# Kernel tuning notes

Measured on AMD Instinct MI355X. Metric: run time of the kernel, lower is better.

The kernel has to match this reference:

```python
import jax, jax.numpy as jnp
import numpy as np

T, B, D, H, NQ = 512, 256, 256, 256, 4  # note H == B is required by the original torch broadcasting


def setup_inputs() -> dict:
    key = jax.random.key(0)
    ks = jax.random.split(key, 9)
    inp = {"inputs": jax.random.normal(ks[0], (T, B, D), jnp.float32)}
    names = ["forget", "input", "update", "output"]
    for j, n in enumerate(names):
        inp[f"W_{n}"] = jax.random.normal(ks[1 + j], (NQ, D + H), jnp.float32) * 0.05
        inp[f"b_{n}"] = jnp.zeros((NQ,), jnp.float32)
        inp[f"phi_{n}"] = jax.random.uniform(ks[5 + j], (NQ,), jnp.float32, 0.0, 2.0 * np.pi)
    return inp


def _qgate(z, phi):
    # 4-qubit circuit on |0000>: RX(z_j) then trainable RX(phi_j) on each wire
    # (two RX on the same wire compose: angle theta_j = z_j + phi_j), then the
    # CNOT ring (0->1,1->2,2->3,3->0), then <Z_0>.
    # Heisenberg picture: conjugating Z_0 back through the CNOT ring gives
    # Z_0 -> Z_1 Z_2 Z_3, and on the product state <Z_j> = cos(theta_j), so
    # <Z_0> = cos(theta_1) * cos(theta_2) * cos(theta_3)  (wire 0 drops out).
    c = jnp.cos(z + phi)  # [B, 4]
    return c[:, 1] * c[:, 2] * c[:, 3]  # [B]


def reference(inputs, W_forget, b_forget, phi_forget, W_input, b_input, phi_input,
              W_update, b_update, phi_update, W_output, b_output, phi_output):
    bsz = inputs.shape[1]
    hx = jnp.zeros((bsz, H), inputs.dtype)
    cx = jnp.zeros((bsz, H), inputs.dtype)

    def step(carry, x):
        hx, cx = carry
        comb = jnp.concatenate([x, hx], axis=1)  # [B, D+H]
        f = jax.nn.sigmoid(_qgate(comb @ W_forget.T + b_forget, phi_forget))   # [B]
        i = jax.nn.sigmoid(_qgate(comb @ W_input.T + b_input, phi_input))      # [B]
        g = jnp.tanh(_qgate(comb @ W_update.T + b_update, phi_update))         # [B]
        o = jax.nn.sigmoid(_qgate(comb @ W_output.T + b_output, phi_output))   # [B]
        # [B] * [B,H] broadcasts the gate over the hidden axis (valid since H == B,
        # exactly matching the original torch semantics)
        cx = f * cx + i * g
        hx = o * jnp.tanh(cx)
        return (hx, cx), hx

    (hx, cx), outs = jax.lax.scan(step, (hx, cx), inputs)
    return outs, hx, cx
```

## Files before the change

kernel.cpp:

```cpp
#include <hip/hip_runtime.h>


#define T_DIM 512
#define B_DIM 256
#define D_DIM 256
#define H_DIM 256
#define DH    512
#define NG    16
#define XPAD  68
#define INV2PI 0.15915494309189535f

typedef float f32x4 __attribute__((ext_vector_type(4)));

__device__ __forceinline__ float fast_sigmoid(float x) {
    return 1.0f / (1.0f + __expf(-x));
}
__device__ __forceinline__ float fast_tanh(float x) {
    float e = __expf(2.0f * x);
    return (e - 1.0f) / (e + 1.0f);
}
__device__ __forceinline__ float cos_rev(float x) {
#if __has_builtin(__builtin_amdgcn_fractf) && __has_builtin(__builtin_amdgcn_cosf)
    return __builtin_amdgcn_cosf(__builtin_amdgcn_fractf(x));
#else
    return __cosf(x * 6.283185307179586f);
#endif
}
template <int CTRL, int RM, int BM, bool BC>
__device__ __forceinline__ float dadd(float x) {
    return x + __int_as_float(
        __builtin_amdgcn_update_dpp(0, __float_as_int(x), CTRL, RM, BM, BC));
}
__device__ __forceinline__ float rsum32(float x) {
    x = dadd<0x111, 0xf, 0xf, true >(x);
    x = dadd<0x112, 0xf, 0xf, true >(x);
    x = dadd<0x114, 0xf, 0xf, true >(x);
    x = dadd<0x118, 0xf, 0xf, true >(x);
    x = dadd<0x142, 0xa, 0xf, false>(x);
    return x;
}
__device__ __forceinline__ float dpp_xor1(float x) {
    return __int_as_float(
        __builtin_amdgcn_update_dpp(0, __float_as_int(x), 0xB1, 0xf, 0xf, true));
}
__device__ __forceinline__ void lds_barrier() {
    __asm__ volatile("s_waitcnt lgkmcnt(0)\n\ts_barrier" ::: "memory");
}

__global__ __launch_bounds__(256) void zx_kernel(
    const float* __restrict__ x,
    const float* __restrict__ Wf, const float* __restrict__ Wi,
    const float* __restrict__ Wu, const float* __restrict__ Wo,
    const float* __restrict__ bf, const float* __restrict__ bi,
    const float* __restrict__ bu, const float* __restrict__ bo,
    const float* __restrict__ phf, const float* __restrict__ phi,
    const float* __restrict__ phu, const float* __restrict__ pho,
    float* __restrict__ zx)
{
    __shared__ float Xc[256][XPAD];
    __shared__ float Wc[NG][XPAD];
    const int tid = threadIdx.x;
    const int rt  = tid >> 2;
    const int qt  = tid & 3;

    const float* bv = (qt == 0) ? bf : (qt == 1) ? bi : (qt == 2) ? bu : bo;
    const float* pv = (qt == 0) ? phf : (qt == 1) ? phi : (qt == 2) ? phu : pho;
    float acc[4][4];
    #pragma unroll
    for (int j = 0; j < 4; ++j) {
        const float bj = bv[j] + pv[j];
        acc[0][j] = bj; acc[1][j] = bj; acc[2][j] = bj; acc[3][j] = bj;
    }

    const long base = (long)blockIdx.x * 256 * D_DIM;

    for (int c = 0; c < 4; ++c) {
        const int k0 = c * 64;
        #pragma unroll
        for (int it = 0; it < 16; ++it) {
            const int e = tid + it * 256;
            const int row = e >> 4, col4 = (e & 15) * 4;
            *(float4*)&Xc[row][col4] =
                *(const float4*)(x + base + (long)row * D_DIM + k0 + col4);
        }
        {
            const int q16 = tid >> 4, col4 = (tid & 15) * 4;
            const int g = q16 >> 2, qj = q16 & 3;
            const float* W = (g == 0) ? Wf : (g == 1) ? Wi : (g == 2) ? Wu : Wo;
            *(float4*)&Wc[q16][col4] = *(const float4*)(W + qj * DH + k0 + col4);
        }
        __syncthreads();

        #pragma unroll 4
        for (int kk = 0; kk < 16; ++kk) {
            const int k4 = kk * 4;
            float4 xv0 = *(float4*)&Xc[rt][k4];
            float4 xv1 = *(float4*)&Xc[rt +  64][k4];
            float4 xv2 = *(float4*)&Xc[rt + 128][k4];
            float4 xv3 = *(float4*)&Xc[rt + 192][k4];
            float4 wv0 = *(float4*)&Wc[4 * qt + 0][k4];
            float4 wv1 = *(float4*)&Wc[4 * qt + 1][k4];
            float4 wv2 = *(float4*)&Wc[4 * qt + 2][k4];
            float4 wv3 = *(float4*)&Wc[4 * qt + 3][k4];
            #pragma unroll
            for (int i = 0; i < 4; ++i) {
                const float4 xv = (i == 0) ? xv0 : (i == 1) ? xv1 : (i == 2) ? xv2 : xv3;
                acc[i][0] = fmaf(xv.x, wv0.x, fmaf(xv.y, wv0.y, fmaf(xv.z, wv0.z, fmaf(xv.w, wv0.w, acc[i][0]))));
                acc[i][1] = fmaf(xv.x, wv1.x, fmaf(xv.y, wv1.y, fmaf(xv.z, wv1.z, fmaf(xv.w, wv1.w, acc[i][1]))));
                acc[i][2] = fmaf(xv.x, wv2.x, fmaf(xv.y, wv2.y, fmaf(xv.z, wv2.z, fmaf(xv.w, wv2.w, acc[i][2]))));
                acc[i][3] = fmaf(xv.x, wv3.x, fmaf(xv.y, wv3.y, fmaf(xv.z, wv3.z, fmaf(xv.w, wv3.w, acc[i][3]))));
            }
        }
        __syncthreads();
    }

    const long orow = (long)blockIdx.x * 256;
    #pragma unroll
    for (int i = 0; i < 4; ++i) {
        *(float4*)&zx[(orow + rt + 64 * i) * NG + qt * 4] =
            make_float4(acc[i][0] * INV2PI, acc[i][1] * INV2PI,
                        acc[i][2] * INV2PI, acc[i][3] * INV2PI);
    }
}

__global__ __launch_bounds__(512) void rec_kernel(
    const float* __restrict__ Wf, const float* __restrict__ Wi,
    const float* __restrict__ Wu, const float* __restrict__ Wo,
    const float* __restrict__ zx,
    float* __restrict__ hv_tab,
    float* __restrict__ c_fin)
{
    __shared__ float Hbuf[2][H_DIM];
    __shared__ __align__(16) float zh_s[2][8];
    const int tid  = threadIdx.x;
    const int lane = tid & 63;
    const int wv   = tid >> 6;
    const int h    = tid >> 1;
    const int half = tid & 1;
    const int l31  = lane & 31;

    float4 W0 = make_float4(0,0,0,0), W1 = W0;
    if (wv < 6) {
        const int c = 2 * wv + (lane >> 5);
        const int g = c / 3, j = c % 3 + 1;
        const float* Wg = (g == 0) ? Wf : (g == 1) ? Wi : (g == 2) ? Wu : Wo;
        W0 = *(const float4*)(Wg + j * DH + 256 + 4 * l31);
        W1 = *(const float4*)(Wg + j * DH + 256 + 128 + 4 * l31);
        W0.x *= INV2PI; W0.y *= INV2PI; W0.z *= INV2PI; W0.w *= INV2PI;
        W1.x *= INV2PI; W1.y *= INV2PI; W1.z *= INV2PI; W1.w *= INV2PI;
    }

    float C = 0.0f, Hprev = 0.0f;
    if (tid < H_DIM) Hbuf[1][tid] = 0.0f;
    __syncthreads();

    float4 za0, za1, zb0, zb1;
    {
        const float4* p0 = (const float4*)(zx + (long)h * NG) + half * 2;
        const float4* p1 = (const float4*)(zx + ((long)B_DIM + h) * NG) + half * 2;
        za0 = p0[0]; za1 = p0[1];
        zb0 = p1[0]; zb1 = p1[1];
    }

    auto step = [&](int t, float4& z0, float4& z1) {
        if (half) hv_tab[(long)(t - 1) * H_DIM + h] = Hprev;

        if (wv < 6) {
            const float4 H0 = *(const float4*)&Hbuf[(t + 1) & 1][4 * l31];
            const float4 H1 = *(const float4*)&Hbuf[(t + 1) & 1][4 * l31 + 128];
            float p0 = fmaf(W0.x, H0.x, fmaf(W0.y, H0.y, fmaf(W0.z, H0.z, W0.w * H0.w)));
            float p1 = fmaf(W1.x, H1.x, fmaf(W1.y, H1.y, fmaf(W1.z, H1.z, W1.w * H1.w)));
            float p  = rsum32(p0 + p1);
            if (l31 == 31) {
                const int c = 2 * wv + (lane >> 5);
                zh_s[c / 6][c % 6] = p;
            }
        }
        lds_barrier();

        const float4 ZA = *(const float4*)&zh_s[half][0];
        const float2 ZB = *(const float2*)&zh_s[half][4];
        const float c1 = cos_rev(z0.y + ZA.x), c2 = cos_rev(z0.z + ZA.y), c3 = cos_rev(z0.w + ZA.z);
        const float c4 = cos_rev(z1.y + ZA.w), c5 = cos_rev(z1.z + ZB.x), c6 = cos_rev(z1.w + ZB.y);
        const float pA = c1 * c2 * c3, pB = c4 * c5 * c6;
        float gA, gB;
        if (half == 0) { gA = fast_sigmoid(pA); gB = fast_sigmoid(pB); }
        else           { gA = fast_tanh(pA);    gB = fast_sigmoid(pB); }
        const float oA = dpp_xor1(gA);
        const float oB = dpp_xor1(gB);
        const float f_ = half ? oA : gA;
        const float i_ = half ? oB : gB;
        const float g_ = half ? gA : oA;
        const float o_ = half ? gB : oB;

        {
            const int tp = (t + 2 < T_DIM) ? (t + 2) : t;
            const float4* pp = (const float4*)(zx + ((long)tp * B_DIM + h) * NG) + half * 2;
            z0 = pp[0]; z1 = pp[1];
        }

        C = fmaf(f_, C, i_ * g_);
        const float Hnew = o_ * fast_tanh(C);
        if (half == 0) Hbuf[t & 1][h] = Hnew;
        Hprev = Hnew;
        lds_barrier();
    };

    for (int t = 0; t < T_DIM; t += 2) {
        step(t,     za0, za1);
        step(t + 1, zb0, zb1);
    }

    if (half) {
        hv_tab[(long)(T_DIM - 1) * H_DIM + h] = Hprev;
        c_fin[h] = C;
    }
}

__global__ __launch_bounds__(256) void bc_kernel(
    const float* __restrict__ hv_tab, const float* __restrict__ c_fin,
    float* __restrict__ out)
{
    const int blk  = blockIdx.x;
    const int w    = threadIdx.x >> 6;
    const int lane = threadIdx.x & 63;

    const float* src;
    long base;
    int rbase;
    if (blk < 4 * T_DIM) {
        const int t = blk >> 2;
        rbase = (blk & 3) * 64;
        src = hv_tab + (long)t * H_DIM;
        base = (long)t * (B_DIM * H_DIM);
    } else {
        const int k = blk - 4 * T_DIM;
        rbase = (k & 3) * 64;
        src = (k < 4) ? (hv_tab + (long)(T_DIM - 1) * H_DIM) : c_fin;
        base = (long)T_DIM * (B_DIM * H_DIM) + (k < 4 ? 0 : (long)B_DIM * H_DIM);
    }
    const f32x4 v = ((const f32x4*)src)[lane];
    #pragma unroll
    for (int it = 0; it < 16; ++it) {
        const int row = rbase + w + 4 * it;
        __builtin_nontemporal_store(
            v, (f32x4*)(out + base + (long)row * H_DIM) + lane);
    }
}

extern "C" void kernel_launch(void* const* d_in, const int* in_sizes, int n_in,
                              void* d_out, int out_size, void* d_ws, size_t ws_size,
                              hipStream_t stream) {
    (void)in_sizes; (void)n_in; (void)out_size; (void)ws_size;
    const float* x   = (const float*)d_in[0];
    const float* Wf  = (const float*)d_in[1];
    const float* bf  = (const float*)d_in[2];
    const float* phf = (const float*)d_in[3];
    const float* Wi  = (const float*)d_in[4];
    const float* bi  = (const float*)d_in[5];
    const float* phi = (const float*)d_in[6];
    const float* Wu  = (const float*)d_in[7];
    const float* bu  = (const float*)d_in[8];
    const float* phu = (const float*)d_in[9];
    const float* Wo  = (const float*)d_in[10];
    const float* bo  = (const float*)d_in[11];
    const float* pho = (const float*)d_in[12];

    float* zx     = (float*)d_ws;
    float* hv_pad = zx + (size_t)T_DIM * B_DIM * NG;
    float* hv_tab = hv_pad + H_DIM;
    float* c_fin  = hv_tab + (size_t)T_DIM * H_DIM;

    zx_kernel<<<T_DIM, 256, 0, stream>>>(
        x, Wf, Wi, Wu, Wo, bf, bi, bu, bo, phf, phi, phu, pho, zx);

    rec_kernel<<<1, 512, 0, stream>>>(
        Wf, Wi, Wu, Wo, zx, hv_tab, c_fin);

    bc_kernel<<<4 * T_DIM + 8, 256, 0, stream>>>(hv_tab, c_fin, (float*)d_out);
}
```

Before: 578.6 us.

## Compute recurrent gate projections redundantly per wave to drop one barrier per step

The recurrent kernel now runs 256 threads, one per hidden unit. Each wave computes all 12 recurrent dot products itself using full 64-lane DPP reductions and a readlane broadcast. This removes the shared zh staging buffer and the second barrier per timestep, and each thread now evaluates all four gates instead of splitting them across thread pairs. The cost is 12x redundant reduction work in every wave and higher register use for 12 weight vectors and 16 prefetched z values.

```diff
diff --git a/kernel.cpp b/kernel.cpp
--- a/kernel.cpp
+++ b/kernel.cpp
@@ -12,6 +12,12 @@
 
 typedef float f32x4 __attribute__((ext_vector_type(4)));
 
+#if __has_builtin(__builtin_amdgcn_fractf) && __has_builtin(__builtin_amdgcn_cosf)
+#define TRIG_REV 1
+#else
+#define TRIG_REV 0
+#endif
+
 __device__ __forceinline__ float fast_sigmoid(float x) {
     return 1.0f / (1.0f + __expf(-x));
 }
@@ -20,7 +26,7 @@
     return (e - 1.0f) / (e + 1.0f);
 }
 __device__ __forceinline__ float cos_rev(float x) {
-#if __has_builtin(__builtin_amdgcn_fractf) && __has_builtin(__builtin_amdgcn_cosf)
+#if TRIG_REV
     return __builtin_amdgcn_cosf(__builtin_amdgcn_fractf(x));
 #else
     return __cosf(x * 6.283185307179586f);
@@ -31,17 +37,17 @@
     return x + __int_as_float(
         __builtin_amdgcn_update_dpp(0, __float_as_int(x), CTRL, RM, BM, BC));
 }
-__device__ __forceinline__ float rsum32(float x) {
+__device__ __forceinline__ float wsum(float x) {
     x = dadd<0x111, 0xf, 0xf, true >(x);
     x = dadd<0x112, 0xf, 0xf, true >(x);
     x = dadd<0x114, 0xf, 0xf, true >(x);
     x = dadd<0x118, 0xf, 0xf, true >(x);
     x = dadd<0x142, 0xa, 0xf, false>(x);
+    x = dadd<0x143, 0xc, 0xf, false>(x);
     return x;
 }
-__device__ __forceinline__ float dpp_xor1(float x) {
-    return __int_as_float(
-        __builtin_amdgcn_update_dpp(0, __float_as_int(x), 0xB1, 0xf, 0xf, true));
+__device__ __forceinline__ float bcast63(float x) {
+    return __int_as_float(__builtin_amdgcn_readlane(__float_as_int(x), 63));
 }
 __device__ __forceinline__ void lds_barrier() {
     __asm__ volatile("s_waitcnt lgkmcnt(0)\n\ts_barrier" ::: "memory");
@@ -123,7 +129,7 @@
     }
 }
 
-__global__ __launch_bounds__(512) void rec_kernel(
+__global__ __launch_bounds__(256) void rec_kernel(
     const float* __restrict__ Wf, const float* __restrict__ Wi,
     const float* __restrict__ Wu, const float* __restrict__ Wo,
     const float* __restrict__ zx,
@@ -131,90 +137,72 @@
     float* __restrict__ c_fin)
 {
     __shared__ float Hbuf[2][H_DIM];
-    __shared__ __align__(16) float zh_s[2][8];
     const int tid  = threadIdx.x;
     const int lane = tid & 63;
-    const int wv   = tid >> 6;
-    const int h    = tid >> 1;
-    const int half = tid & 1;
-    const int l31  = lane & 31;
-
-    float4 W0 = make_float4(0,0,0,0), W1 = W0;
-    if (wv < 6) {
-        const int c = 2 * wv + (lane >> 5);
+    const int h    = tid;
+
+    float4 W[12];
+    #pragma unroll
+    for (int c = 0; c < 12; ++c) {
         const int g = c / 3, j = c % 3 + 1;
         const float* Wg = (g == 0) ? Wf : (g == 1) ? Wi : (g == 2) ? Wu : Wo;
-        W0 = *(const float4*)(Wg + j * DH + 256 + 4 * l31);
-        W1 = *(const float4*)(Wg + j * DH + 256 + 128 + 4 * l31);
-        W0.x *= INV2PI; W0.y *= INV2PI; W0.z *= INV2PI; W0.w *= INV2PI;
-        W1.x *= INV2PI; W1.y *= INV2PI; W1.z *= INV2PI; W1.w *= INV2PI;
+        float4 w = *(const float4*)(Wg + j * DH + 256 + 4 * lane);
+        w.x *= INV2PI; w.y *= INV2PI; w.z *= INV2PI; w.w *= INV2PI;
+        W[c] = w;
     }
 
     float C = 0.0f, Hprev = 0.0f;
-    if (tid < H_DIM) Hbuf[1][tid] = 0.0f;
+    Hbuf[1][tid] = 0.0f;
     __syncthreads();
 
-    float4 za0, za1, zb0, zb1;
+    float4 za0, za1, za2, za3, zb0, zb1, zb2, zb3;
     {
-        const float4* p0 = (const float4*)(zx + (long)h * NG) + half * 2;
-        const float4* p1 = (const float4*)(zx + ((long)B_DIM + h) * NG) + half * 2;
-        za0 = p0[0]; za1 = p0[1];
-        zb0 = p1[0]; zb1 = p1[1];
-    }
-
-    auto step = [&](int t, float4& z0, float4& z1) {
-        if (half) hv_tab[(long)(t - 1) * H_DIM + h] = Hprev;
-
-        if (wv < 6) {
-            const float4 H0 = *(const float4*)&Hbuf[(t + 1) & 1][4 * l31];
-            const float4 H1 = *(const float4*)&Hbuf[(t + 1) & 1][4 * l31 + 128];
-            float p0 = fmaf(W0.x, H0.x, fmaf(W0.y, H0.y, fmaf(W0.z, H0.z, W0.w * H0.w)));
-            float p1 = fmaf(W1.x, H1.x, fmaf(W1.y, H1.y, fmaf(W1.z, H1.z, W1.w * H1.w)));
-            float p  = rsum32(p0 + p1);
-            if (l31 == 31) {
-                const int c = 2 * wv + (lane >> 5);
-                zh_s[c / 6][c % 6] = p;
-            }
-        }
-        lds_barrier();
-
-        const float4 ZA = *(const float4*)&zh_s[half][0];
-        const float2 ZB = *(const float2*)&zh_s[half][4];
-        const float c1 = cos_rev(z0.y + ZA.x), c2 = cos_rev(z0.z + ZA.y), c3 = cos_rev(z0.w + ZA.z);
-        const float c4 = cos_rev(z1.y + ZA.w), c5 = cos_rev(z1.z + ZB.x), c6 = cos_rev(z1.w + ZB.y);
-        const float pA = c1 * c2 * c3, pB = c4 * c5 * c6;
-        float gA, gB;
-        if (half == 0) { gA = fast_sigmoid(pA); gB = fast_sigmoid(pB); }
-        else           { gA = fast_tanh(pA);    gB = fast_sigmoid(pB); }
-        const float oA = dpp_xor1(gA);
-        const float oB = dpp_xor1(gB);
-        const float f_ = half ? oA : gA;
-        const float i_ = half ? oB : gB;
-        const float g_ = half ? gA : oA;
-        const float o_ = half ? gB : oB;
-
+        const float4* p0 = (const float4*)(zx + (long)h * NG);
+        const float4* p1 = (const float4*)(zx + ((long)B_DIM + h) * NG);
+        za0 = p0[0]; za1 = p0[1]; za2 = p0[2]; za3 = p0[3];
+        zb0 = p1[0]; zb1 = p1[1]; zb2 = p1[2]; zb3 = p1[3];
+    }
+
+    auto step = [&](int t, float4& z0, float4& z1, float4& z2, float4& z3) {
+        const float4 Hv4 = *(const float4*)&Hbuf[(t + 1) & 1][4 * lane];
+        hv_tab[(long)(t - 1) * H_DIM + h] = Hprev;
+
+        float p[12];
+        #pragma unroll
+        for (int c = 0; c < 12; ++c)
+            p[c] = fmaf(W[c].x, Hv4.x, fmaf(W[c].y, Hv4.y,
+                       fmaf(W[c].z, Hv4.z, W[c].w * Hv4.w)));
+        float zh[12];
+        #pragma unroll
+        for (int c = 0; c < 12; ++c) zh[c] = bcast63(wsum(p[c]));
+
+        float4 n0, n1, n2, n3;
         {
             const int tp = (t + 2 < T_DIM) ? (t + 2) : t;
-            const float4* pp = (const float4*)(zx + ((long)tp * B_DIM + h) * NG) + half * 2;
-            z0 = pp[0]; z1 = pp[1];
-        }
+            const float4* pp = (const float4*)(zx + ((long)tp * B_DIM + h) * NG);
+            n0 = pp[0]; n1 = pp[1]; n2 = pp[2]; n3 = pp[3];
+        }
+
+        const float f_ = fast_sigmoid(cos_rev(z0.y + zh[0]) * cos_rev(z0.z + zh[1])  * cos_rev(z0.w + zh[2]));
+        const float i_ = fast_sigmoid(cos_rev(z1.y + zh[3]) * cos_rev(z1.z + zh[4])  * cos_rev(z1.w + zh[5]));
+        const float g_ = fast_tanh   (cos_rev(z2.y + zh[6]) * cos_rev(z2.z + zh[7])  * cos_rev(z2.w + zh[8]));
+        const float o_ = fast_sigmoid(cos_rev(z3.y + zh[9]) * cos_rev(z3.z + zh[10]) * cos_rev(z3.w + zh[11]));
 
         C = fmaf(f_, C, i_ * g_);
         const float Hnew = o_ * fast_tanh(C);
-        if (half == 0) Hbuf[t & 1][h] = Hnew;
+        Hbuf[t & 1][h] = Hnew;
         Hprev = Hnew;
+        z0 = n0; z1 = n1; z2 = n2; z3 = n3;
         lds_barrier();
     };
 
     for (int t = 0; t < T_DIM; t += 2) {
-        step(t,     za0, za1);
-        step(t + 1, zb0, zb1);
-    }
-
-    if (half) {
-        hv_tab[(long)(T_DIM - 1) * H_DIM + h] = Hprev;
-        c_fin[h] = C;
-    }
+        step(t,     za0, za1, za2, za3);
+        step(t + 1, zb0, zb1, zb2, zb3);
+    }
+
+    hv_tab[(long)(T_DIM - 1) * H_DIM + h] = Hprev;
+    c_fin[h] = C;
 }
 
 __global__ __launch_bounds__(256) void bc_kernel(
@@ -274,7 +262,7 @@
     zx_kernel<<<T_DIM, 256, 0, stream>>>(
         x, Wf, Wi, Wu, Wo, bf, bi, bu, bo, phf, phi, phu, pho, zx);
 
-    rec_kernel<<<1, 512, 0, stream>>>(
+    rec_kernel<<<1, 256, 0, stream>>>(
         Wf, Wi, Wu, Wo, zx, hv_tab, c_fin);
 
     bc_kernel<<<4 * T_DIM + 8, 256, 0, stream>>>(hv_tab, c_fin, (float*)d_out);
```

Result: slower. 639.3 us (+10.5%).
